# Kernel tuning notes

Hardware: AMD Instinct MI355X
Metric: run time of the kernel (lower is better)

Reference implementation:

```python
import jax, jax.numpy as jnp
import numpy as np

N = 2048   # nodes per graph
M = 64     # input feature dim (m)
H = 256    # hidden_dim
E = 65536  # directed edges per graph
B = 8      # batch of graphs
EPS = 1e-5


def setup_inputs() -> dict:
    key = jax.random.key(0)
    ks = jax.random.split(key, 24)
    def xavier(k, out_d, in_d):
        s = float(np.sqrt(6.0 / (in_d + out_d)))
        return jax.random.uniform(k, (out_d, in_d), minval=-s, maxval=s, dtype=jnp.float32)
    dims = [(H, M), (2 * H, H), (4 * H, 2 * H), (4 * H, 4 * H), (4 * H, 4 * H)]
    inp = {}
    for i, (o, ii) in enumerate(dims, start=1):
        inp[f"w{i}"] = xavier(ks[i], o, ii)
        inp[f"b{i}"] = jnp.zeros((o,), jnp.float32)
        inp[f"g{i}"] = jnp.ones((o,), jnp.float32)   # batchnorm gamma
        inp[f"be{i}"] = jnp.zeros((o,), jnp.float32)  # batchnorm beta
    inp["ln_g"] = jnp.ones((4 * H,), jnp.float32)
    inp["ln_b"] = jnp.zeros((4 * H,), jnp.float32)
    inp["x"] = jax.random.normal(ks[20], (B, N, M, 1), dtype=jnp.float32)
    inp["edge_index"] = jax.random.randint(ks[21], (2, E), 0, N, dtype=jnp.int64)
    return inp


def reference(x, edge_index,
              w1, b1, g1, be1,
              w2, b2, g2, be2,
              w3, b3, g3, be3,
              w4, b4, g4, be4,
              w5, b5, g5, be5,
              ln_g, ln_b):
    # GCN normalization with self-loops (PyG GCNConv default), shared across batch
    loop = jnp.arange(N, dtype=edge_index.dtype)
    src = jnp.concatenate([edge_index[0], loop])
    dst = jnp.concatenate([edge_index[1], loop])
    deg = jax.ops.segment_sum(jnp.ones(src.shape[0], jnp.float32), dst, num_segments=N)
    dinv = deg ** -0.5
    norm = (dinv[src] * dinv[dst])[:, None]  # [E+N, 1]

    def gcn(h, w, b):
        h = h @ w.T                                        # [N, out]
        agg = jax.ops.segment_sum(h[src] * norm, dst, num_segments=N)
        return agg + b

    def bn(h, g, be):  # batchnorm over nodes (training stats, biased var)
        mu = h.mean(axis=0)
        var = ((h - mu) ** 2).mean(axis=0)
        return (h - mu) * jax.lax.rsqrt(var + EPS) * g + be

    def layer(h, w, b, g, be):
        return bn(jax.nn.leaky_relu(gcn(h, w, b), 0.01), g, be)

    def per_graph(xg):  # xg: [N, M, 1]
        h = xg[..., 0]
        h = layer(h, w1, b1, g1, be1)
        h = layer(h, w2, b2, g2, be2)
        h = layer(h, w3, b3, g3, be3)
        h = layer(h, w4, b4, g4, be4)
        h = layer(h, w5, b5, g5, be5)
        mu = h.mean(axis=-1, keepdims=True)
        var = ((h - mu) ** 2).mean(axis=-1, keepdims=True)
        h = (h - mu) * jax.lax.rsqrt(var + EPS) * ln_g + ln_b
        return h.reshape(-1)  # [N * 4H]

    return jax.vmap(per_graph)(x)  # [B, N*4H]
```

## Files before the change

kernel.cpp:

```cpp
#include <hip/hip_runtime.h>

#define NN 2048
#define EE 65536
#define BB 8
#define EPSF 1e-5f

typedef __attribute__((ext_vector_type(4))) float f32x4;
typedef __attribute__((ext_vector_type(4))) int i32x4;
typedef __attribute__((ext_vector_type(8))) short short8;
typedef __attribute__((ext_vector_type(4))) unsigned short u16x4;

__device__ inline unsigned short f2bf(float f) {
    unsigned u = __float_as_uint(f);
    unsigned r = (u + 0x7fffu + ((u >> 16) & 1u)) >> 16;
    return (unsigned short)r;
}
__device__ inline float bf2f(unsigned short u) {
    return __uint_as_float(((unsigned)u) << 16);
}

__device__ inline void gload16(const unsigned short* g, unsigned short* l) {
    __builtin_amdgcn_global_load_lds(
        (const __attribute__((address_space(1))) void*)g,
        (__attribute__((address_space(3))) void*)l, 16, 0, 0);
}

__global__ void zero_i32(int* p, int n) {
    int i = blockIdx.x * 256 + threadIdx.x;
    if (i < n) p[i] = 0;
}
__global__ void zero_f32(float* p, int n) {
    int i = blockIdx.x * 256 + threadIdx.x;
    if (i < n) p[i] = 0.f;
}

__global__ void count_kernel(const int* __restrict__ ei, int* __restrict__ counts) {
    int e = blockIdx.x * 256 + threadIdx.x;
    if (e < EE + NN) {
        int d = (e < EE) ? ei[EE + e] : (e - EE);
        atomicAdd(&counts[d], 1);
    }
}

__global__ void dinv_kernel(const int* __restrict__ counts, float* __restrict__ dinv) {
    int i = blockIdx.x * 256 + threadIdx.x;
    if (i < NN) dinv[i] = rsqrtf((float)counts[i]);
}

__global__ void scan_kernel(const int* __restrict__ counts, int* __restrict__ row_ptr) {
    __shared__ int sh[256];
    int tid = threadIdx.x;
    int loc[8];
    int run = 0;
#pragma unroll
    for (int i = 0; i < 8; ++i) {
        loc[i] = run;
        run += (counts[tid * 8 + i] + 3) & ~3;
    }
    sh[tid] = run;
    __syncthreads();
    for (int off = 1; off < 256; off <<= 1) {
        int v = (tid >= off) ? sh[tid - off] : 0;
        __syncthreads();
        sh[tid] += v;
        __syncthreads();
    }
    int excl = sh[tid] - run;
#pragma unroll
    for (int i = 0; i < 8; ++i) row_ptr[tid * 8 + i] = excl + loc[i];
    if (tid == 255) row_ptr[NN] = excl + run;
}

__global__ void fill_kernel(const int* __restrict__ ei, const float* __restrict__ dinv,
                            const int* __restrict__ row_ptr, int* __restrict__ fillc,
                            int* __restrict__ colA, float* __restrict__ valA) {
    int e = blockIdx.x * 256 + threadIdx.x;
    if (e < EE + NN) {
        int s, d;
        if (e < EE) { s = ei[e]; d = ei[EE + e]; }
        else        { s = d = e - EE; }
        int pos = row_ptr[d] + atomicAdd(&fillc[d], 1);
        colA[pos] = s;
        valA[pos] = dinv[s] * dinv[d];
    }
}

__global__ void pad_kernel(const int* __restrict__ counts, const int* __restrict__ row_ptr,
                           int* __restrict__ colA, float* __restrict__ valA) {
    int d = blockIdx.x * 256 + threadIdx.x;
    if (d < NN) {
        int beg = row_ptr[d], end = row_ptr[d + 1];
        for (int k = counts[d]; k < end - beg; ++k) {
            colA[beg + k] = d;
            valA[beg + k] = 0.f;
        }
    }
}

__global__ void rowsum_kernel(const int* __restrict__ row_ptr, const float* __restrict__ valA,
                              float* __restrict__ R) {
    int d = blockIdx.x * 256 + threadIdx.x;
    if (d < NN) {
        float s = 0.f;
        for (int j = row_ptr[d]; j < row_ptr[d + 1]; ++j) s += valA[j];
        R[d] = s;
    }
}

__global__ void conv_bf16(const float* __restrict__ src, unsigned short* __restrict__ dst, int n) {
    int i = blockIdx.x * 256 + threadIdx.x;
    if (i < n) dst[i] = f2bf(src[i]);
}

__global__ __launch_bounds__(256) void agg_f32(
    const float* __restrict__ Yin, const int* __restrict__ row_ptr,
    const int* __restrict__ colA, const float* __restrict__ valA,
    unsigned short* __restrict__ Aout) {
    constexpr int TPD = 16, DPB = 16, F = 64;
    int b = blockIdx.x & 7;
    int dst = (blockIdx.x >> 3) * DPB + threadIdx.x / TPD;
    int lane = threadIdx.x % TPD;
    const f32x4* Yb = (const f32x4*)(Yin + (size_t)b * NN * F);
    int beg = row_ptr[dst], end = row_ptr[dst + 1];
    f32x4 acc = {0.f, 0.f, 0.f, 0.f};
    for (int j = beg; j < end; j += 4) {
        i32x4 c4 = *(const i32x4*)(colA + j);
        f32x4 v4 = *(const f32x4*)(valA + j);
        f32x4 y0 = Yb[(size_t)c4[0] * (F / 4) + lane];
        f32x4 y1 = Yb[(size_t)c4[1] * (F / 4) + lane];
        f32x4 y2 = Yb[(size_t)c4[2] * (F / 4) + lane];
        f32x4 y3 = Yb[(size_t)c4[3] * (F / 4) + lane];
        acc += v4[0] * y0;
        acc += v4[1] * y1;
        acc += v4[2] * y2;
        acc += v4[3] * y3;
    }
    u16x4 ob = {f2bf(acc[0]), f2bf(acc[1]), f2bf(acc[2]), f2bf(acc[3])};
    *(u16x4*)(Aout + (size_t)b * NN * F + (size_t)dst * F + lane * 4) = ob;
}

template <int TPD>
__global__ __launch_bounds__(256) void agg_bf16(
    const unsigned short* __restrict__ Yin, const int* __restrict__ row_ptr,
    const int* __restrict__ colA, const float* __restrict__ valA,
    const float* __restrict__ rowsumR, const float* __restrict__ s_arr,
    const float* __restrict__ t_arr, unsigned short* __restrict__ Aout, int F) {
    constexpr int DPB = 256 / TPD;
    int b = blockIdx.x & 7;
    int dst = (blockIdx.x >> 3) * DPB + threadIdx.x / TPD;
    int lane = threadIdx.x % TPD;
    const unsigned short* Yb = Yin + (size_t)b * NN * F;
    int beg = row_ptr[dst], end = row_ptr[dst + 1];
    float acc[8] = {};
    for (int j = beg; j < end; j += 4) {
        i32x4 c4 = *(const i32x4*)(colA + j);
        f32x4 v4 = *(const f32x4*)(valA + j);
        short8 y0 = *(const short8*)(Yb + (size_t)c4[0] * F + lane * 8);
        short8 y1 = *(const short8*)(Yb + (size_t)c4[1] * F + lane * 8);
        short8 y2 = *(const short8*)(Yb + (size_t)c4[2] * F + lane * 8);
        short8 y3 = *(const short8*)(Yb + (size_t)c4[3] * F + lane * 8);
#pragma unroll
        for (int k = 0; k < 8; ++k) {
            acc[k] += v4[0] * bf2f((unsigned short)y0[k]);
            acc[k] += v4[1] * bf2f((unsigned short)y1[k]);
            acc[k] += v4[2] * bf2f((unsigned short)y2[k]);
            acc[k] += v4[3] * bf2f((unsigned short)y3[k]);
        }
    }
    float R = rowsumR[dst];
    f32x4 s0 = ((const f32x4*)(s_arr + b * F))[lane * 2];
    f32x4 s1 = ((const f32x4*)(s_arr + b * F))[lane * 2 + 1];
    f32x4 t0 = ((const f32x4*)(t_arr + b * F))[lane * 2];
    f32x4 t1 = ((const f32x4*)(t_arr + b * F))[lane * 2 + 1];
    unsigned short ob[8];
#pragma unroll
    for (int k = 0; k < 4; ++k) ob[k] = f2bf(s0[k] * acc[k] + t0[k] * R);
#pragma unroll
    for (int k = 0; k < 4; ++k) ob[4 + k] = f2bf(s1[k] * acc[4 + k] + t1[k] * R);
    *(short8*)(Aout + (size_t)b * NN * F + (size_t)dst * F + lane * 8) = *(short8*)ob;
}

__global__ __launch_bounds__(256) void gemm_bias_lrelu(
    const unsigned short* __restrict__ A, const unsigned short* __restrict__ W,
    const float* __restrict__ bias, unsigned short* __restrict__ Y,
    float* __restrict__ bnsum, float* __restrict__ bnsq, int K, int F) {
    __shared__ unsigned short lds_a[128 * 32];
    __shared__ unsigned short lds_b[128 * 32];
    const int tid = threadIdx.x;
    const int row0 = blockIdx.x * 128;
    const int col0 = blockIdx.y * 128;
    const int b = row0 >> 11;
    const int wave = tid >> 6;
    const int lane = tid & 63;
    const int wr = (wave >> 1) * 64;
    const int wc = (wave & 1) * 64;
    const int lrow = lane & 15;
    const int q = lane >> 4;
    const int lr = lane >> 2;
    const int lk = (lane & 3) * 8;

    f32x4 acc[4][4] = {};

    for (int k0 = 0; k0 < K; k0 += 32) {
#pragma unroll
        for (int t = 0; t < 2; ++t) {
            int r = wave * 32 + t * 16;
            gload16(A + (size_t)(row0 + r + lr) * K + k0 + lk, lds_a + r * 32);
            gload16(W + (size_t)(col0 + r + lr) * K + k0 + lk, lds_b + r * 32);
        }
        __syncthreads();
        short8 af[4], bf[4];
#pragma unroll
        for (int mt = 0; mt < 4; ++mt)
            af[mt] = *(const short8*)(lds_a + (wr + mt * 16 + lrow) * 32 + q * 8);
#pragma unroll
        for (int nt = 0; nt < 4; ++nt)
            bf[nt] = *(const short8*)(lds_b + (wc + nt * 16 + lrow) * 32 + q * 8);
#pragma unroll
        for (int mt = 0; mt < 4; ++mt)
#pragma unroll
            for (int nt = 0; nt < 4; ++nt)
                acc[mt][nt] = __builtin_amdgcn_mfma_f32_16x16x32_bf16(af[mt], bf[nt], acc[mt][nt], 0, 0, 0);
        __syncthreads();
    }
#pragma unroll
    for (int nt = 0; nt < 4; ++nt) {
        int col = col0 + wc + nt * 16 + lrow;
        float bv = bias[col];
        float s = 0.f, s2 = 0.f;
#pragma unroll
        for (int mt = 0; mt < 4; ++mt) {
#pragma unroll
            for (int reg = 0; reg < 4; ++reg) {
                int row = row0 + wr + mt * 16 + q * 4 + reg;
                float v = acc[mt][nt][reg] + bv;
                v = (v > 0.f) ? v : 0.01f * v;
                s += v;
                s2 += v * v;
                Y[(size_t)row * F + col] = f2bf(v);
            }
        }
        s += __shfl_xor(s, 16);
        s2 += __shfl_xor(s2, 16);
        s += __shfl_xor(s, 32);
        s2 += __shfl_xor(s2, 32);
        if (q == 0) {
            atomicAdd(&bnsum[b * F + col], s);
            atomicAdd(&bnsq[b * F + col], s2);
        }
    }
}

__global__ void bn_finalize(const float* __restrict__ sum, const float* __restrict__ sq,
                            const float* __restrict__ g, const float* __restrict__ be,
                            float* __restrict__ s_arr, float* __restrict__ t_arr, int F) {
    int i = blockIdx.x * 256 + threadIdx.x;
    if (i >= BB * F) return;
    int c = i % F;
    float mu = sum[i] * (1.f / NN);
    float var = sq[i] * (1.f / NN) - mu * mu;
    float rs = rsqrtf(var + EPSF);
    float sc = g[c] * rs;
    s_arr[i] = sc;
    t_arr[i] = be[c] - mu * sc;
}

__global__ __launch_bounds__(256) void final_ln(const unsigned short* __restrict__ Y,
                                                const float* __restrict__ s_arr, const float* __restrict__ t_arr,
                                                const float* __restrict__ lng, const float* __restrict__ lnb,
                                                float* __restrict__ out) {
    int bn = blockIdx.x;
    int b = bn >> 11;
    int tid = threadIdx.x;
    u16x4 hr = ((const u16x4*)(Y + (size_t)bn * 1024))[tid];
    f32x4 h = {bf2f(hr[0]), bf2f(hr[1]), bf2f(hr[2]), bf2f(hr[3])};
    f32x4 sv = ((const f32x4*)(s_arr + b * 1024))[tid];
    f32x4 tv = ((const f32x4*)(t_arr + b * 1024))[tid];
    h = sv * h + tv;
    float s = h[0] + h[1] + h[2] + h[3];
    float s2 = h[0] * h[0] + h[1] * h[1] + h[2] * h[2] + h[3] * h[3];
#pragma unroll
    for (int off = 32; off; off >>= 1) {
        s += __shfl_down(s, off);
        s2 += __shfl_down(s2, off);
    }
    __shared__ float ssum[4], ssq[4];
    int wv = tid >> 6, ln = tid & 63;
    if (ln == 0) { ssum[wv] = s; ssq[wv] = s2; }
    __syncthreads();
    if (tid == 0) {
        float S = ssum[0] + ssum[1] + ssum[2] + ssum[3];
        float Q = ssq[0] + ssq[1] + ssq[2] + ssq[3];
        float mu = S * (1.f / 1024.f);
        float var = Q * (1.f / 1024.f) - mu * mu;
        ssum[0] = mu;
        ssq[0] = rsqrtf(var + EPSF);
    }
    __syncthreads();
    float mu = ssum[0], rs = ssq[0];
    f32x4 gv = ((const f32x4*)lng)[tid];
    f32x4 bv = ((const f32x4*)lnb)[tid];
    f32x4 o = (h - mu) * rs * gv + bv;
    ((f32x4*)(out + (size_t)bn * 1024))[tid] = o;
}

extern "C" void kernel_launch(void* const* d_in, const int* in_sizes, int n_in,
                              void* d_out, int out_size, void* d_ws, size_t ws_size,
                              hipStream_t stream) {
    const float* w[5]    = {(const float*)d_in[0], (const float*)d_in[4], (const float*)d_in[8],
                            (const float*)d_in[12], (const float*)d_in[16]};
    const float* bias[5] = {(const float*)d_in[1], (const float*)d_in[5], (const float*)d_in[9],
                            (const float*)d_in[13], (const float*)d_in[17]};
    const float* gam[5]  = {(const float*)d_in[2], (const float*)d_in[6], (const float*)d_in[10],
                            (const float*)d_in[14], (const float*)d_in[18]};
    const float* bet[5]  = {(const float*)d_in[3], (const float*)d_in[7], (const float*)d_in[11],
                            (const float*)d_in[15], (const float*)d_in[19]};
    const float* ln_g = (const float*)d_in[20];
    const float* ln_b = (const float*)d_in[21];
    const float* x    = (const float*)d_in[22];
    const int* ei     = (const int*)d_in[23];

    char* p = (char*)d_ws;
    auto alloc = [&](size_t bytes) {
        char* r = p;
        p += (bytes + 255) & ~(size_t)255;
        return r;
    };
    const int MAXE = EE + 4 * NN;
    float* dinv    = (float*)alloc(NN * 4);
    float* rowsumR = (float*)alloc(NN * 4);
    int* row_ptr   = (int*)alloc((NN + 1) * 4);
    int* counts    = (int*)alloc(NN * 4);
    int* fillc     = (int*)alloc(NN * 4);
    int* colA      = (int*)alloc((size_t)MAXE * 4);
    float* valA    = (float*)alloc((size_t)MAXE * 4);
    float* bnsum   = (float*)alloc((size_t)5 * BB * 1024 * 4);
    float* bnsq    = (float*)alloc((size_t)5 * BB * 1024 * 4);
    float* s_arr   = (float*)alloc((size_t)BB * 1024 * 4);
    float* t_arr   = (float*)alloc((size_t)BB * 1024 * 4);
    const int wsz[5] = {256 * 64, 512 * 256, 1024 * 512, 1024 * 1024, 1024 * 1024};
    unsigned short* wbf[5];
    for (int i = 0; i < 5; ++i) wbf[i] = (unsigned short*)alloc((size_t)wsz[i] * 2);
    unsigned short* bufA = (unsigned short*)alloc((size_t)BB * NN * 1024 * 2);
    unsigned short* bufY = (unsigned short*)alloc((size_t)BB * NN * 1024 * 2);

    zero_i32<<<(NN + 255) / 256, 256, 0, stream>>>(counts, NN);
    zero_i32<<<(NN + 255) / 256, 256, 0, stream>>>(fillc, NN);
    zero_f32<<<(5 * BB * 1024 + 255) / 256, 256, 0, stream>>>(bnsum, 5 * BB * 1024);
    zero_f32<<<(5 * BB * 1024 + 255) / 256, 256, 0, stream>>>(bnsq, 5 * BB * 1024);
    count_kernel<<<(EE + NN + 255) / 256, 256, 0, stream>>>(ei, counts);
    dinv_kernel<<<(NN + 255) / 256, 256, 0, stream>>>(counts, dinv);
    scan_kernel<<<1, 256, 0, stream>>>(counts, row_ptr);
    fill_kernel<<<(EE + NN + 255) / 256, 256, 0, stream>>>(ei, dinv, row_ptr, fillc, colA, valA);
    pad_kernel<<<(NN + 255) / 256, 256, 0, stream>>>(counts, row_ptr, colA, valA);
    rowsum_kernel<<<(NN + 255) / 256, 256, 0, stream>>>(row_ptr, valA, rowsumR);

    for (int i = 0; i < 5; ++i)
        conv_bf16<<<(wsz[i] + 255) / 256, 256, 0, stream>>>(w[i], wbf[i], wsz[i]);

    const int Kin[5]  = {64, 256, 512, 1024, 1024};
    const int Fout[5] = {256, 512, 1024, 1024, 1024};
    for (int l = 0; l < 5; ++l) {
        int K = Kin[l], F = Fout[l];
        if (l == 0) {
            agg_f32<<<(NN / 16) * 8, 256, 0, stream>>>(x, row_ptr, colA, valA, bufA);
        } else {
            switch (K) {
                case 256:
                    agg_bf16<32><<<(NN / 8) * 8, 256, 0, stream>>>(bufY, row_ptr, colA, valA, rowsumR, s_arr, t_arr, bufA, K);
                    break;
                case 512:
                    agg_bf16<64><<<(NN / 4) * 8, 256, 0, stream>>>(bufY, row_ptr, colA, valA, rowsumR, s_arr, t_arr, bufA, K);
                    break;
                default:
                    agg_bf16<128><<<(NN / 2) * 8, 256, 0, stream>>>(bufY, row_ptr, colA, valA, rowsumR, s_arr, t_arr, bufA, K);
                    break;
            }
        }
        gemm_bias_lrelu<<<dim3(BB * NN / 128, F / 128), 256, 0, stream>>>(
            bufA, wbf[l], bias[l], bufY, bnsum + l * BB * 1024, bnsq + l * BB * 1024, K, F);
        bn_finalize<<<(BB * F + 255) / 256, 256, 0, stream>>>(
            bnsum + l * BB * 1024, bnsq + l * BB * 1024, gam[l], bet[l], s_arr, t_arr, F);
    }
    final_ln<<<BB * NN, 256, 0, stream>>>(bufY, s_arr, t_arr, ln_g, ln_b, (float*)d_out);
}
```

Measured before the change: 571.8 us.

## Merge setup kernels, unroll aggregation to 8 edges, use packed f32x2 math

Merges the four zeroing kernels into one launch, fuses fill with padding, and converts all five weight matrices in a single launch. This cuts the number of small kernel launches. The aggregation kernels now pad rows to multiples of 8 and process 8 neighbours per iteration, giving more loads in flight. The bf16 unpack uses 32-bit word shifts and packed f32x2 FMAs, with the feature width as a template constant. Padding to 8 adds more zero-weight edges that are loaded and computed but contribute nothing.

```diff
diff --git a/kernel.cpp b/kernel.cpp
--- a/kernel.cpp
+++ b/kernel.cpp
@@ -5,8 +5,10 @@
 #define BB 8
 #define EPSF 1e-5f
 
+typedef __attribute__((ext_vector_type(2))) float f32x2;
 typedef __attribute__((ext_vector_type(4))) float f32x4;
 typedef __attribute__((ext_vector_type(4))) int i32x4;
+typedef __attribute__((ext_vector_type(4))) unsigned int u32x4;
 typedef __attribute__((ext_vector_type(8))) short short8;
 typedef __attribute__((ext_vector_type(4))) unsigned short u16x4;
 
@@ -25,13 +27,11 @@
         (__attribute__((address_space(3))) void*)l, 16, 0, 0);
 }
 
-__global__ void zero_i32(int* p, int n) {
+__global__ void setup_zero(int* __restrict__ counts, int* __restrict__ fillc,
+                           float* __restrict__ bnsum, float* __restrict__ bnsq) {
     int i = blockIdx.x * 256 + threadIdx.x;
-    if (i < n) p[i] = 0;
-}
-__global__ void zero_f32(float* p, int n) {
-    int i = blockIdx.x * 256 + threadIdx.x;
-    if (i < n) p[i] = 0.f;
+    if (i < NN) { counts[i] = 0; fillc[i] = 0; }
+    if (i < 5 * BB * 1024) { bnsum[i] = 0.f; bnsq[i] = 0.f; }
 }
 
 __global__ void count_kernel(const int* __restrict__ ei, int* __restrict__ counts) {
@@ -55,7 +55,7 @@
 #pragma unroll
     for (int i = 0; i < 8; ++i) {
         loc[i] = run;
-        run += (counts[tid * 8 + i] + 3) & ~3;
+        run += (counts[tid * 8 + i] + 7) & ~7;
     }
     sh[tid] = run;
     __syncthreads();
@@ -71,9 +71,9 @@
     if (tid == 255) row_ptr[NN] = excl + run;
 }
 
-__global__ void fill_kernel(const int* __restrict__ ei, const float* __restrict__ dinv,
-                            const int* __restrict__ row_ptr, int* __restrict__ fillc,
-                            int* __restrict__ colA, float* __restrict__ valA) {
+__global__ void fill_pad(const int* __restrict__ ei, const float* __restrict__ dinv,
+                         const int* __restrict__ row_ptr, const int* __restrict__ counts,
+                         int* __restrict__ fillc, int* __restrict__ colA, float* __restrict__ valA) {
     int e = blockIdx.x * 256 + threadIdx.x;
     if (e < EE + NN) {
         int s, d;
@@ -82,13 +82,8 @@
         int pos = row_ptr[d] + atomicAdd(&fillc[d], 1);
         colA[pos] = s;
         valA[pos] = dinv[s] * dinv[d];
-    }
-}
-
-__global__ void pad_kernel(const int* __restrict__ counts, const int* __restrict__ row_ptr,
-                           int* __restrict__ colA, float* __restrict__ valA) {
-    int d = blockIdx.x * 256 + threadIdx.x;
-    if (d < NN) {
+    } else if (e < EE + 2 * NN) {
+        int d = e - (EE + NN);
         int beg = row_ptr[d], end = row_ptr[d + 1];
         for (int k = counts[d]; k < end - beg; ++k) {
             colA[beg + k] = d;
@@ -107,9 +102,23 @@
     }
 }
 
-__global__ void conv_bf16(const float* __restrict__ src, unsigned short* __restrict__ dst, int n) {
+#define WO1 16384
+#define WO2 (WO1 + 131072)
+#define WO3 (WO2 + 524288)
+#define WO4 (WO3 + 1048576)
+#define WO5 (WO4 + 1048576)
+__global__ void conv_all(const float* __restrict__ s0, const float* __restrict__ s1,
+                         const float* __restrict__ s2, const float* __restrict__ s3,
+                         const float* __restrict__ s4, unsigned short* __restrict__ dst) {
     int i = blockIdx.x * 256 + threadIdx.x;
-    if (i < n) dst[i] = f2bf(src[i]);
+    if (i >= WO5) return;
+    float v;
+    if (i < WO1)      v = s0[i];
+    else if (i < WO2) v = s1[i - WO1];
+    else if (i < WO3) v = s2[i - WO2];
+    else if (i < WO4) v = s3[i - WO3];
+    else              v = s4[i - WO4];
+    dst[i] = f2bf(v);
 }
 
 __global__ __launch_bounds__(256) void agg_f32(
@@ -123,60 +132,69 @@
     const f32x4* Yb = (const f32x4*)(Yin + (size_t)b * NN * F);
     int beg = row_ptr[dst], end = row_ptr[dst + 1];
     f32x4 acc = {0.f, 0.f, 0.f, 0.f};
-    for (int j = beg; j < end; j += 4) {
-        i32x4 c4 = *(const i32x4*)(colA + j);
-        f32x4 v4 = *(const f32x4*)(valA + j);
-        f32x4 y0 = Yb[(size_t)c4[0] * (F / 4) + lane];
-        f32x4 y1 = Yb[(size_t)c4[1] * (F / 4) + lane];
-        f32x4 y2 = Yb[(size_t)c4[2] * (F / 4) + lane];
-        f32x4 y3 = Yb[(size_t)c4[3] * (F / 4) + lane];
-        acc += v4[0] * y0;
-        acc += v4[1] * y1;
-        acc += v4[2] * y2;
-        acc += v4[3] * y3;
+    for (int j = beg; j < end; j += 8) {
+        i32x4 ca = *(const i32x4*)(colA + j);
+        i32x4 cb = *(const i32x4*)(colA + j + 4);
+        f32x4 va = *(const f32x4*)(valA + j);
+        f32x4 vb = *(const f32x4*)(valA + j + 4);
+        f32x4 y[8];
+#pragma unroll
+        for (int e = 0; e < 4; ++e) y[e] = Yb[(size_t)ca[e] * (F / 4) + lane];
+#pragma unroll
+        for (int e = 0; e < 4; ++e) y[4 + e] = Yb[(size_t)cb[e] * (F / 4) + lane];
+#pragma unroll
+        for (int e = 0; e < 8; ++e) {
+            float ve = (e < 4) ? va[e] : vb[e - 4];
+            acc += ve * y[e];
+        }
     }
     u16x4 ob = {f2bf(acc[0]), f2bf(acc[1]), f2bf(acc[2]), f2bf(acc[3])};
     *(u16x4*)(Aout + (size_t)b * NN * F + (size_t)dst * F + lane * 4) = ob;
 }
 
-template <int TPD>
+template <int F>
 __global__ __launch_bounds__(256) void agg_bf16(
     const unsigned short* __restrict__ Yin, const int* __restrict__ row_ptr,
     const int* __restrict__ colA, const float* __restrict__ valA,
     const float* __restrict__ rowsumR, const float* __restrict__ s_arr,
-    const float* __restrict__ t_arr, unsigned short* __restrict__ Aout, int F) {
+    const float* __restrict__ t_arr, unsigned short* __restrict__ Aout) {
+    constexpr int TPD = F / 8;
     constexpr int DPB = 256 / TPD;
     int b = blockIdx.x & 7;
     int dst = (blockIdx.x >> 3) * DPB + threadIdx.x / TPD;
     int lane = threadIdx.x % TPD;
-    const unsigned short* Yb = Yin + (size_t)b * NN * F;
+    const u32x4* Yb4 = (const u32x4*)(Yin + (size_t)b * NN * F);
     int beg = row_ptr[dst], end = row_ptr[dst + 1];
-    float acc[8] = {};
-    for (int j = beg; j < end; j += 4) {
-        i32x4 c4 = *(const i32x4*)(colA + j);
-        f32x4 v4 = *(const f32x4*)(valA + j);
-        short8 y0 = *(const short8*)(Yb + (size_t)c4[0] * F + lane * 8);
-        short8 y1 = *(const short8*)(Yb + (size_t)c4[1] * F + lane * 8);
-        short8 y2 = *(const short8*)(Yb + (size_t)c4[2] * F + lane * 8);
-        short8 y3 = *(const short8*)(Yb + (size_t)c4[3] * F + lane * 8);
-#pragma unroll
-        for (int k = 0; k < 8; ++k) {
-            acc[k] += v4[0] * bf2f((unsigned short)y0[k]);
-            acc[k] += v4[1] * bf2f((unsigned short)y1[k]);
-            acc[k] += v4[2] * bf2f((unsigned short)y2[k]);
-            acc[k] += v4[3] * bf2f((unsigned short)y3[k]);
+    f32x2 acc[4] = {};
+    for (int j = beg; j < end; j += 8) {
+        i32x4 ca = *(const i32x4*)(colA + j);
+        i32x4 cb = *(const i32x4*)(colA + j + 4);
+        f32x4 va = *(const f32x4*)(valA + j);
+        f32x4 vb = *(const f32x4*)(valA + j + 4);
+        u32x4 y[8];
+#pragma unroll
+        for (int e = 0; e < 4; ++e) y[e] = Yb4[(size_t)ca[e] * (F / 8) + lane];
+#pragma unroll
+        for (int e = 0; e < 4; ++e) y[4 + e] = Yb4[(size_t)cb[e] * (F / 8) + lane];
+#pragma unroll
+        for (int e = 0; e < 8; ++e) {
+            float ve = (e < 4) ? va[e] : vb[e - 4];
+            f32x2 vv = {ve, ve};
+#pragma unroll
+            for (int d = 0; d < 4; ++d) {
+                unsigned w = y[e][d];
+                f32x2 f = {__uint_as_float(w << 16), __uint_as_float(w & 0xffff0000u)};
+                acc[d] += vv * f;
+            }
         }
     }
     float R = rowsumR[dst];
-    f32x4 s0 = ((const f32x4*)(s_arr + b * F))[lane * 2];
-    f32x4 s1 = ((const f32x4*)(s_arr + b * F))[lane * 2 + 1];
-    f32x4 t0 = ((const f32x4*)(t_arr + b * F))[lane * 2];
-    f32x4 t1 = ((const f32x4*)(t_arr + b * F))[lane * 2 + 1];
+    const float* sb = s_arr + b * F + lane * 8;
+    const float* tb = t_arr + b * F + lane * 8;
     unsigned short ob[8];
 #pragma unroll
-    for (int k = 0; k < 4; ++k) ob[k] = f2bf(s0[k] * acc[k] + t0[k] * R);
-#pragma unroll
-    for (int k = 0; k < 4; ++k) ob[4 + k] = f2bf(s1[k] * acc[4 + k] + t1[k] * R);
+    for (int k = 0; k < 8; ++k)
+        ob[k] = f2bf(sb[k] * acc[k >> 1][k & 1] + tb[k] * R);
     *(short8*)(Aout + (size_t)b * NN * F + (size_t)dst * F + lane * 8) = *(short8*)ob;
 }
 
@@ -326,7 +344,7 @@
         p += (bytes + 255) & ~(size_t)255;
         return r;
     };
-    const int MAXE = EE + 4 * NN;
+    const int MAXE = EE + 8 * NN;
     float* dinv    = (float*)alloc(NN * 4);
     float* rowsumR = (float*)alloc(NN * 4);
     int* row_ptr   = (int*)alloc((NN + 1) * 4);
@@ -338,25 +356,18 @@
     float* bnsq    = (float*)alloc((size_t)5 * BB * 1024 * 4);
     float* s_arr   = (float*)alloc((size_t)BB * 1024 * 4);
     float* t_arr   = (float*)alloc((size_t)BB * 1024 * 4);
-    const int wsz[5] = {256 * 64, 512 * 256, 1024 * 512, 1024 * 1024, 1024 * 1024};
-    unsigned short* wbf[5];
-    for (int i = 0; i < 5; ++i) wbf[i] = (unsigned short*)alloc((size_t)wsz[i] * 2);
+    unsigned short* wbf = (unsigned short*)alloc((size_t)WO5 * 2);
     unsigned short* bufA = (unsigned short*)alloc((size_t)BB * NN * 1024 * 2);
     unsigned short* bufY = (unsigned short*)alloc((size_t)BB * NN * 1024 * 2);
-
-    zero_i32<<<(NN + 255) / 256, 256, 0, stream>>>(counts, NN);
-    zero_i32<<<(NN + 255) / 256, 256, 0, stream>>>(fillc, NN);
-    zero_f32<<<(5 * BB * 1024 + 255) / 256, 256, 0, stream>>>(bnsum, 5 * BB * 1024);
-    zero_f32<<<(5 * BB * 1024 + 255) / 256, 256, 0, stream>>>(bnsq, 5 * BB * 1024);
+    const int wofs[5] = {0, WO1, WO2, WO3, WO4};
+
+    setup_zero<<<(5 * BB * 1024 + 255) / 256, 256, 0, stream>>>(counts, fillc, bnsum, bnsq);
     count_kernel<<<(EE + NN + 255) / 256, 256, 0, stream>>>(ei, counts);
     dinv_kernel<<<(NN + 255) / 256, 256, 0, stream>>>(counts, dinv);
     scan_kernel<<<1, 256, 0, stream>>>(counts, row_ptr);
-    fill_kernel<<<(EE + NN + 255) / 256, 256, 0, stream>>>(ei, dinv, row_ptr, fillc, colA, valA);
-    pad_kernel<<<(NN + 255) / 256, 256, 0, stream>>>(counts, row_ptr, colA, valA);
+    fill_pad<<<(EE + 2 * NN + 255) / 256, 256, 0, stream>>>(ei, dinv, row_ptr, counts, fillc, colA, valA);
     rowsum_kernel<<<(NN + 255) / 256, 256, 0, stream>>>(row_ptr, valA, rowsumR);
-
-    for (int i = 0; i < 5; ++i)
-        conv_bf16<<<(wsz[i] + 255) / 256, 256, 0, stream>>>(w[i], wbf[i], wsz[i]);
+    conv_all<<<(WO5 + 255) / 256, 256, 0, stream>>>(w[0], w[1], w[2], w[3], w[4], wbf);
 
     const int Kin[5]  = {64, 256, 512, 1024, 1024};
     const int Fout[5] = {256, 512, 1024, 1024, 1024};
@@ -367,18 +378,18 @@
         } else {
             switch (K) {
                 case 256:
-                    agg_bf16<32><<<(NN / 8) * 8, 256, 0, stream>>>(bufY, row_ptr, colA, valA, rowsumR, s_arr, t_arr, bufA, K);
+                    agg_bf16<256><<<(NN / 8) * 8, 256, 0, stream>>>(bufY, row_ptr, colA, valA, rowsumR, s_arr, t_arr, bufA);
                     break;
                 case 512:
-                    agg_bf16<64><<<(NN / 4) * 8, 256, 0, stream>>>(bufY, row_ptr, colA, valA, rowsumR, s_arr, t_arr, bufA, K);
+                    agg_bf16<512><<<(NN / 4) * 8, 256, 0, stream>>>(bufY, row_ptr, colA, valA, rowsumR, s_arr, t_arr, bufA);
                     break;
                 default:
-                    agg_bf16<128><<<(NN / 2) * 8, 256, 0, stream>>>(bufY, row_ptr, colA, valA, rowsumR, s_arr, t_arr, bufA, K);
+                    agg_bf16<1024><<<(NN / 2) * 8, 256, 0, stream>>>(bufY, row_ptr, colA, valA, rowsumR, s_arr, t_arr, bufA);
                     break;
             }
         }
         gemm_bias_lrelu<<<dim3(BB * NN / 128, F / 128), 256, 0, stream>>>(
-            bufA, wbf[l], bias[l], bufY, bnsum + l * BB * 1024, bnsq + l * BB * 1024, K, F);
+            bufA, wbf + wofs[l], bias[l], bufY, bnsum + l * BB * 1024, bnsq + l * BB * 1024, K, F);
         bn_finalize<<<(BB * F + 255) / 256, 256, 0, stream>>>(
             bnsum + l * BB * 1024, bnsq + l * BB * 1024, gam[l], bet[l], s_arr, t_arr, F);
     }
```

Result: faster. 551.7 us (-3.5%).
